# Optimization experiments

Measured on AMD Instinct MI355X. Metric: run time of the kernel, lower is better.

The kernel has to match this reference:

```python
import jax, jax.numpy as jnp
import numpy as np

B, S, D, H = 2, 2048, 1024, 16
DK = D // H
ALPHA = 0.5


def setup_inputs() -> dict:
    key = jax.random.key(0)
    ks = jax.random.split(key, 16)
    scale = 0.02
    return {
        "q": jax.random.normal(ks[0], (B, S, D), dtype=jnp.float32),
        "k": jax.random.normal(ks[1], (B, S, D), dtype=jnp.float32),
        "v": jax.random.normal(ks[2], (B, S, D), dtype=jnp.float32),
        "attn_mask": jax.random.randint(ks[3], (S, S), 0, 2, dtype=jnp.int32),
        "causal_mask": jax.random.uniform(ks[4], (S, S), dtype=jnp.float32),
        "Wq": jax.random.normal(ks[5], (D, D), dtype=jnp.float32) * scale,
        "bq": jnp.zeros((D,), dtype=jnp.float32),
        "Wk": jax.random.normal(ks[6], (D, D), dtype=jnp.float32) * scale,
        "bk": jnp.zeros((D,), dtype=jnp.float32),
        "Wv": jax.random.normal(ks[7], (D, D), dtype=jnp.float32) * scale,
        "bv": jnp.zeros((D,), dtype=jnp.float32),
        "Wo": jax.random.normal(ks[8], (D, D), dtype=jnp.float32) * scale,
        "bo": jnp.zeros((D,), dtype=jnp.float32),
    }


def _split_heads(x):
    # [B, S, D] -> [B, H, S, DK]
    return x.reshape(B, S, H, DK).transpose(0, 2, 1, 3)


def reference(q, k, v, attn_mask, causal_mask, Wq, bq, Wk, bk, Wv, bv, Wo, bo):
    qh = _split_heads(q @ Wq.T + bq)
    kh = _split_heads(k @ Wk.T + bk)
    vh = _split_heads(v @ Wv.T + bv)
    scores = jnp.einsum("bhqd,bhkd->bhqk", qh, kh) / jnp.sqrt(jnp.float32(DK))
    # additive mask: positions where attn_mask == 1 get -1e9 (broadcast [S,S] -> [B,H,S,S])
    scores = jnp.where(attn_mask[None, None] == 1, jnp.float32(-1e9), scores)
    # multiplicative causal scaling (applied AFTER the fill, as in the original)
    scores = scores * (1.0 + ALPHA * causal_mask[None, None])
    probs = jax.nn.softmax(scores, axis=-1)  # dropout is identity in eval / p=0
    attn = jnp.einsum("bhqk,bhkd->bhqd", probs, vh)  # [B, H, S, DK]
    concat = attn.transpose(0, 2, 1, 3).reshape(B, S, D)
    out = concat @ Wo.T + bo
    return (out, attn)
```

## Files before the change

### kernel.cpp

```cpp
#include <hip/hip_runtime.h>
#include <hip/hip_bf16.h>

#define NB 2
#define NS 2048
#define ND 1024
#define NH 16
#define NDK 64
#define GK 1024

using bf16_t = __hip_bfloat16;
typedef __attribute__((ext_vector_type(8))) short bf16x8;
typedef __attribute__((ext_vector_type(4))) float f32x4;
typedef unsigned short u16;
typedef unsigned int u32;

#define SC_LOG2E 0.1803368801f

static __device__ __forceinline__ u16 f2bf(float f) {
    __hip_bfloat16 h = __float2bfloat16(f);
    return *reinterpret_cast<u16*>(&h);
}

static __device__ __forceinline__ u32 cvtpk2(float a, float b) {
    u32 r;
    asm("v_cvt_pk_bf16_f32 %0, %1, %2" : "=v"(r) : "v"(a), "v"(b));
    return r;
}

#define GLDS16(gp, lp)                                                                    \
    __builtin_amdgcn_global_load_lds((const __attribute__((address_space(1))) void*)(gp), \
                                     (__attribute__((address_space(3))) void*)(lp), 16, 0, 0)

struct PrepArgs {
    const float* qkv_s[3];
    u16* qkv_d[3];
    const float* w_s[4];
    u16* w_d[4];
    const int* am;
    const float* cm;
    float* comb;
};

__global__ __launch_bounds__(256) void prep_kernel(PrepArgs a) {
    const int x = blockIdx.x, y = blockIdx.y, tid = threadIdx.x;
    if (y < 3) {
        int i = x * 256 + tid;
        float4 v = reinterpret_cast<const float4*>(a.qkv_s[y])[i];
        ushort4 o;
        o.x = f2bf(v.x); o.y = f2bf(v.y); o.z = f2bf(v.z); o.w = f2bf(v.w);
        reinterpret_cast<ushort4*>(a.qkv_d[y])[i] = o;
    } else if (y == 3) {
        int w = x >> 10;
        int i = (x & 1023) * 256 + tid;
        float4 v = reinterpret_cast<const float4*>(a.w_s[w])[i];
        ushort4 o;
        o.x = f2bf(v.x); o.y = f2bf(v.y); o.z = f2bf(v.z); o.w = f2bf(v.w);
        reinterpret_cast<ushort4*>(a.w_d[w])[i] = o;
    } else {
        int i = (x * 256 + tid) * 4;
        int4 m = *reinterpret_cast<const int4*>(a.am + i);
        float4 c = *reinterpret_cast<const float4*>(a.cm + i);
        float4 r;
        r.x = (m.x == 1) ? -1.0f : fmaf(0.5f * SC_LOG2E, c.x, SC_LOG2E);
        r.y = (m.y == 1) ? -1.0f : fmaf(0.5f * SC_LOG2E, c.y, SC_LOG2E);
        r.z = (m.z == 1) ? -1.0f : fmaf(0.5f * SC_LOG2E, c.z, SC_LOG2E);
        r.w = (m.w == 1) ? -1.0f : fmaf(0.5f * SC_LOG2E, c.w, SC_LOG2E);
        *reinterpret_cast<float4*>(a.comb + i) = r;
    }
}

struct MMArgs {
    const u16* A;
    const u16* W;
    const float* bias;
    void* out;
};

template <int BN, int MODE>
__global__ __launch_bounds__(256) void mm_glds(MMArgs g0, MMArgs g1, MMArgs g2) {
    const MMArgs ga = (blockIdx.z == 0) ? g0 : (blockIdx.z == 1) ? g1 : g2;
    constexpr int BM = 128, BK = 32;
    constexpr int JN = BN / 32;
    __shared__ __align__(16) u16 As[2][BM * BK];
    __shared__ __align__(16) u16 Bs[2][BN * BK];

    const int tid = threadIdx.x;
    const int lane = tid & 63;
    const int w = tid >> 6;
    const int wm = w >> 1, wn = w & 1;
    const int fr = lane & 15, fg = lane >> 4;
    const int bm0 = blockIdx.y * BM, bn0 = blockIdx.x * BN;

    const u16* agp = ga.A + (size_t)(bm0 + w * 32 + (lane >> 2)) * GK + (lane & 3) * 8;
    const u16* bgp = ga.W +
                     (size_t)(bn0 + w * (BN == 128 ? 32 : 16) + (lane >> 2)) * GK +
                     (lane & 3) * 8;

    f32x4 acc[4][JN];
    const f32x4 z4 = {0.f, 0.f, 0.f, 0.f};
#pragma unroll
    for (int i = 0; i < 4; ++i)
#pragma unroll
        for (int j = 0; j < JN; ++j) acc[i][j] = z4;

    {
        u16* la = &As[0][w * 1024];
        u16* lb = &Bs[0][w * (BN == 128 ? 1024 : 512)];
        GLDS16(agp, la);
        GLDS16(agp + 16 * GK, la + 512);
        if (BN == 128) {
            GLDS16(bgp, lb);
            GLDS16(bgp + 16 * GK, lb + 512);
        } else {
            GLDS16(bgp, lb);
        }
    }
    __syncthreads();

    int cur = 0;
    for (int kt = 0; kt < GK / BK; ++kt) {
        if (kt + 1 < GK / BK) {
            const int ko = (kt + 1) * BK;
            u16* la = &As[cur ^ 1][w * 1024];
            u16* lb = &Bs[cur ^ 1][w * (BN == 128 ? 1024 : 512)];
            GLDS16(agp + ko, la);
            GLDS16(agp + ko + 16 * GK, la + 512);
            if (BN == 128) {
                GLDS16(bgp + ko, lb);
                GLDS16(bgp + ko + 16 * GK, lb + 512);
            } else {
                GLDS16(bgp + ko, lb);
            }
        }
        bf16x8 af[4], bfr[JN];
#pragma unroll
        for (int i = 0; i < 4; ++i)
            af[i] = *(const bf16x8*)&As[cur][(wm * 64 + i * 16 + fr) * BK + fg * 8];
#pragma unroll
        for (int j = 0; j < JN; ++j)
            bfr[j] = *(const bf16x8*)&Bs[cur][(wn * (BN / 2) + j * 16 + fr) * BK + fg * 8];
#pragma unroll
        for (int i = 0; i < 4; ++i)
#pragma unroll
            for (int j = 0; j < JN; ++j)
                acc[i][j] = __builtin_amdgcn_mfma_f32_16x16x32_bf16(af[i], bfr[j], acc[i][j],
                                                                    0, 0, 0);
        __syncthreads();
        cur ^= 1;
    }

#pragma unroll
    for (int j = 0; j < JN; ++j) {
        const int col = bn0 + wn * (BN / 2) + j * 16 + fr;
        const float bv_ = ga.bias[col];
#pragma unroll
        for (int i = 0; i < 4; ++i) {
#pragma unroll
            for (int r = 0; r < 4; ++r) {
                const int row = bm0 + wm * 64 + i * 16 + fg * 4 + r;
                const float val = acc[i][j][r] + bv_;
                if (MODE == 1) {
                    const int b_ = row >> 11, s_ = row & (NS - 1);
                    const int h_ = col >> 6, dk = col & (NDK - 1);
                    ((bf16_t*)ga.out)[(((size_t)(b_ * NH + h_)) * NS + s_) * NDK + dk] =
                        __float2bfloat16(val);
                } else {
                    ((float*)ga.out)[(size_t)row * ND + col] = val;
                }
            }
        }
    }
}

__global__ __launch_bounds__(256) void vtrans_kernel(const u16* __restrict__ Vh,
                                                     u16* __restrict__ VhT) {
    __shared__ __align__(16) u16 T[64][72];
    const int t = threadIdx.x;
    const int bh = blockIdx.y;
    const int s0 = blockIdx.x * 64;
    const size_t boff = (size_t)bh * NS * NDK;

    const int vkp = t & 31;
    const int vdk = (t >> 5) * 8;
    int4 va = *(const int4*)(Vh + boff + (size_t)(s0 + 2 * vkp) * NDK + vdk);
    int4 vb = *(const int4*)(Vh + boff + (size_t)(s0 + 2 * vkp + 1) * NDK + vdk);
    {
        const u16* a = (const u16*)&va;
        const u16* b = (const u16*)&vb;
#pragma unroll
        for (int j = 0; j < 8; ++j) {
            u32 pk = (u32)a[j] | ((u32)b[j] << 16);
            *(u32*)&T[vdk + j][2 * vkp] = pk;
        }
    }
    __syncthreads();
    const int d = t >> 2;
    const int so = (t & 3) * 16;
    int4 o0 = *(const int4*)&T[d][so];
    int4 o1 = *(const int4*)&T[d][so + 8];
    u16* op = VhT + boff + (size_t)d * NS + s0 + so;
    *(int4*)(op) = o0;
    *(int4*)(op + 8) = o1;
}

__global__ __launch_bounds__(256) void flash_mfma(const u16* __restrict__ Qh,
                                                  const u16* __restrict__ Kh,
                                                  const u16* __restrict__ VhT,
                                                  const float* __restrict__ comb,
                                                  float* __restrict__ attnOut,
                                                  u16* __restrict__ concatOut) {
    __shared__ __align__(16) u16 Kt[2][64 * 64];
    __shared__ __align__(16) u16 Vt[2][64 * 64];
    __shared__ __align__(16) u16 Pt[4][16][64];

    const int tid = threadIdx.x;
    const int w = tid >> 6;
    const int lane = tid & 63;
    const int qc = lane & 15;
    const int g = lane >> 4;
    const int bh = blockIdx.y;
    const int b_ = bh >> 4, h_ = bh & 15;
    const int qw = blockIdx.x * 64 + w * 16;

    const size_t bhoff = (size_t)bh * NS * NDK;

    const int srow = lane >> 3;
    const int sblk = (lane & 7) ^ srow;
    const u16* kgp = Kh + bhoff + (size_t)(w * 16 + srow) * NDK + sblk * 8;
    const u16* vgp = VhT + bhoff + (size_t)(w * 16 + srow) * NS + sblk * 8;

    bf16x8 qf[2];
    {
        const u16* qp = Qh + bhoff + (size_t)(qw + qc) * NDK + g * 8;
        qf[0] = *(const bf16x8*)(qp);
        qf[1] = *(const bf16x8*)(qp + 32);
    }

    bf16x8 vones;
#pragma unroll
    for (int j = 0; j < 8; ++j) vones[j] = (short)0x3F80;

    const f32x4 z4 = {0.f, 0.f, 0.f, 0.f};
    f32x4 o[4];
    o[0] = o[1] = o[2] = o[3] = z4;
    f32x4 o_l = z4;

    const float* crow = comb + (size_t)(qw + qc) * NS;
    const int kxor = qc & 7;
    const int pxor = (qc & 7) << 4;
    char* ptrow = (char*)&Pt[w][0][0] + qc * 128;

    {
        u16* kd = &Kt[0][(w * 16) * 64];
        u16* vd = &Vt[0][(w * 16) * 64];
        GLDS16(kgp, kd);
        GLDS16(kgp + 8 * NDK, kd + 512);
        GLDS16(vgp, vd);
        GLDS16(vgp + 8 * NS, vd + 512);
    }
    float4 cpre[4];
#pragma unroll
    for (int ks = 0; ks < 4; ++ks)
        cpre[ks] = *(const float4*)(crow + ks * 16 + g * 4);
    __syncthreads();

    int cur = 0;
#pragma unroll 2
    for (int kt = 0; kt < NS; kt += 64) {
        if (kt + 64 < NS) {
            u16* kd = &Kt[cur ^ 1][(w * 16) * 64];
            u16* vd = &Vt[cur ^ 1][(w * 16) * 64];
            GLDS16(kgp + (kt + 64) * NDK, kd);
            GLDS16(kgp + (kt + 64 + 8) * NDK, kd + 512);
            GLDS16(vgp + (kt + 64), vd);
            GLDS16(vgp + 8 * NS + (kt + 64), vd + 512);
        }
        float4 cc4[4];
#pragma unroll
        for (int ks = 0; ks < 4; ++ks) cc4[ks] = cpre[ks];
        if (kt + 64 < NS) {
#pragma unroll
            for (int ks = 0; ks < 4; ++ks)
                cpre[ks] = *(const float4*)(crow + kt + 64 + ks * 16 + g * 4);
        }

        f32x4 s[4];
        s[0] = s[1] = s[2] = s[3] = z4;
        __builtin_amdgcn_s_setprio(1);
#pragma unroll
        for (int kc = 0; kc < 2; ++kc) {
#pragma unroll
            for (int ks = 0; ks < 4; ++ks) {
                bf16x8 kf = *(const bf16x8*)&Kt[cur][(ks * 16 + qc) * 64 +
                                                     (((kc << 2) | g) ^ kxor) * 8];
                s[ks] = __builtin_amdgcn_mfma_f32_16x16x32_bf16(kf, qf[kc], s[ks], 0, 0, 0);
            }
        }
        __builtin_amdgcn_s_setprio(0);

#pragma unroll
        for (int ks = 0; ks < 4; ++ks) {
            const float* cc = (const float*)&cc4[ks];
            float p0 = __builtin_amdgcn_exp2f(s[ks][0] * cc[0]);
            float p1 = __builtin_amdgcn_exp2f(s[ks][1] * cc[1]);
            float p2 = __builtin_amdgcn_exp2f(s[ks][2] * cc[2]);
            float p3 = __builtin_amdgcn_exp2f(s[ks][3] * cc[3]);
            p0 = (cc[0] < 0.f) ? 0.f : p0;
            p1 = (cc[1] < 0.f) ? 0.f : p1;
            p2 = (cc[2] < 0.f) ? 0.f : p2;
            p3 = (cc[3] < 0.f) ? 0.f : p3;
            uint2 pw;
            pw.x = cvtpk2(p0, p1);
            pw.y = cvtpk2(p2, p3);
            *(uint2*)(ptrow + ((ks * 32 + g * 8) ^ pxor)) = pw;
        }

        __builtin_amdgcn_s_setprio(1);
#pragma unroll
        for (int kc = 0; kc < 2; ++kc) {
            bf16x8 pf = *(const bf16x8*)(ptrow + ((kc * 64 + g * 16) ^ pxor));
            o_l = __builtin_amdgcn_mfma_f32_16x16x32_bf16(pf, vones, o_l, 0, 0, 0);
#pragma unroll
            for (int dsub = 0; dsub < 4; ++dsub) {
                bf16x8 vf = *(const bf16x8*)&Vt[cur][(dsub * 16 + qc) * 64 +
                                                     (((kc << 2) | g) ^ kxor) * 8];
                o[dsub] = __builtin_amdgcn_mfma_f32_16x16x32_bf16(pf, vf, o[dsub], 0, 0, 0);
            }
        }
        __builtin_amdgcn_s_setprio(0);
        __syncthreads();
        cur ^= 1;
    }

    float inv[4];
#pragma unroll
    for (int r = 0; r < 4; ++r) inv[r] = 1.0f / o_l[r];

#pragma unroll
    for (int dsub = 0; dsub < 4; ++dsub) {
#pragma unroll
        for (int r = 0; r < 4; ++r) {
            const float val = o[dsub][r] * inv[r];
            const int qg = qw + g * 4 + r;
            const int d = dsub * 16 + qc;
            attnOut[bhoff + (size_t)qg * NDK + d] = val;
            concatOut[((size_t)b_ * NS + qg) * ND + h_ * NDK + d] = f2bf(val);
        }
    }
}

extern "C" void kernel_launch(void* const* d_in, const int* in_sizes, int n_in,
                              void* d_out, int out_size, void* d_ws, size_t ws_size,
                              hipStream_t stream) {
    const float* q = (const float*)d_in[0];
    const float* k = (const float*)d_in[1];
    const float* v = (const float*)d_in[2];
    const int* am = (const int*)d_in[3];
    const float* cm = (const float*)d_in[4];
    const float* Wq = (const float*)d_in[5];
    const float* bq = (const float*)d_in[6];
    const float* Wk = (const float*)d_in[7];
    const float* bk = (const float*)d_in[8];
    const float* Wv = (const float*)d_in[9];
    const float* bv = (const float*)d_in[10];
    const float* Wo = (const float*)d_in[11];
    const float* bo = (const float*)d_in[12];

    float* out = (float*)d_out;
    float* attn_out = out + (size_t)NB * NS * ND;

    char* p = (char*)d_ws;
    float* CB = (float*)p;  p += (size_t)NS * NS * 4;
    u16* qb = (u16*)p;      p += (size_t)NB * NS * ND * 2;
    u16* kb_ = (u16*)p;     p += (size_t)NB * NS * ND * 2;
    u16* vb_ = (u16*)p;     p += (size_t)NB * NS * ND * 2;
    u16* Wqb = (u16*)p;     p += (size_t)ND * ND * 2;
    u16* Wkb = (u16*)p;     p += (size_t)ND * ND * 2;
    u16* Wvb = (u16*)p;     p += (size_t)ND * ND * 2;
    u16* Wob = (u16*)p;     p += (size_t)ND * ND * 2;
    u16* Qh = (u16*)p;      p += (size_t)NB * NS * ND * 2;
    u16* Kh = (u16*)p;      p += (size_t)NB * NS * ND * 2;
    u16* Vh = (u16*)p;      p += (size_t)NB * NS * ND * 2;
    u16* VhT = (u16*)p;     p += (size_t)NB * NS * ND * 2;
    u16* CCb = (u16*)p;     p += (size_t)NB * NS * ND * 2;

    PrepArgs pa;
    pa.qkv_s[0] = q;  pa.qkv_d[0] = qb;
    pa.qkv_s[1] = k;  pa.qkv_d[1] = kb_;
    pa.qkv_s[2] = v;  pa.qkv_d[2] = vb_;
    pa.w_s[0] = Wq;   pa.w_d[0] = Wqb;
    pa.w_s[1] = Wk;   pa.w_d[1] = Wkb;
    pa.w_s[2] = Wv;   pa.w_d[2] = Wvb;
    pa.w_s[3] = Wo;   pa.w_d[3] = Wob;
    pa.am = am;
    pa.cm = cm;
    pa.comb = CB;
    hipLaunchKernelGGL(prep_kernel, dim3(4096, 5), dim3(256), 0, stream, pa);

    MMArgs mq = {qb, Wqb, bq, (void*)Qh};
    MMArgs mk = {kb_, Wkb, bk, (void*)Kh};
    MMArgs mv = {vb_, Wvb, bv, (void*)Vh};
    hipLaunchKernelGGL((mm_glds<128, 1>), dim3(ND / 128, 4096 / 128, 3), dim3(256), 0, stream,
                       mq, mk, mv);

    hipLaunchKernelGGL(vtrans_kernel, dim3(NS / 64, NB * NH), dim3(256), 0, stream, Vh, VhT);

    hipLaunchKernelGGL(flash_mfma, dim3(NS / 64, NB * NH), dim3(256), 0, stream, Qh, Kh, VhT,
                       CB, attn_out, CCb);

    MMArgs mo = {CCb, Wob, bo, (void*)out};
    hipLaunchKernelGGL((mm_glds<64, 0>), dim3(ND / 64, 4096 / 128, 1), dim3(256), 0, stream,
                       mo, mo, mo);
}
```

Measured before the change: 195.7 us.

## Fuse V transpose into projection epilogue and load V fragments directly from global

The V projection GEMM now writes its output already transposed (per head, dk-major) through a runtime mode flag, so the separate transpose kernel and the Vh buffer go away. The attention kernel drops the shared-memory V tile and loads the V fragments for each key block straight from global memory into registers. It also replaces the prefetched mask registers with direct loads, removes the priority hints, and sets an occupancy hint of 5 blocks per SM. The intent is to save a launch and a round trip through memory for V, and to free LDS and registers for more resident blocks. In exchange, V reads are no longer staged or double-buffered, and the GEMM epilogue now branches on a runtime mode.

```diff
diff --git a/kernel.cpp b/kernel.cpp
--- a/kernel.cpp
+++ b/kernel.cpp
@@ -74,9 +74,10 @@
     const u16* W;
     const float* bias;
     void* out;
+    int mode;
 };
 
-template <int BN, int MODE>
+template <int BN>
 __global__ __launch_bounds__(256) void mm_glds(MMArgs g0, MMArgs g1, MMArgs g2) {
     const MMArgs ga = (blockIdx.z == 0) ? g0 : (blockIdx.z == 1) ? g1 : g2;
     constexpr int BM = 128, BK = 32;
@@ -153,64 +154,46 @@
     for (int j = 0; j < JN; ++j) {
         const int col = bn0 + wn * (BN / 2) + j * 16 + fr;
         const float bv_ = ga.bias[col];
-#pragma unroll
-        for (int i = 0; i < 4; ++i) {
-#pragma unroll
-            for (int r = 0; r < 4; ++r) {
-                const int row = bm0 + wm * 64 + i * 16 + fg * 4 + r;
-                const float val = acc[i][j][r] + bv_;
-                if (MODE == 1) {
-                    const int b_ = row >> 11, s_ = row & (NS - 1);
-                    const int h_ = col >> 6, dk = col & (NDK - 1);
-                    ((bf16_t*)ga.out)[(((size_t)(b_ * NH + h_)) * NS + s_) * NDK + dk] =
-                        __float2bfloat16(val);
-                } else {
-                    ((float*)ga.out)[(size_t)row * ND + col] = val;
+        if (ga.mode == 2) {
+            const int h_ = col >> 6, dk = col & (NDK - 1);
+#pragma unroll
+            for (int i = 0; i < 4; ++i) {
+                const int row0 = bm0 + wm * 64 + i * 16 + fg * 4;
+                const int b_ = row0 >> 11, s_ = row0 & (NS - 1);
+                uint2 pw;
+                pw.x = cvtpk2(acc[i][j][0] + bv_, acc[i][j][1] + bv_);
+                pw.y = cvtpk2(acc[i][j][2] + bv_, acc[i][j][3] + bv_);
+                *(uint2*)((u16*)ga.out +
+                          (((size_t)(b_ * NH + h_)) * NDK + dk) * NS + s_) = pw;
+            }
+        } else {
+#pragma unroll
+            for (int i = 0; i < 4; ++i) {
+#pragma unroll
+                for (int r = 0; r < 4; ++r) {
+                    const int row = bm0 + wm * 64 + i * 16 + fg * 4 + r;
+                    const float val = acc[i][j][r] + bv_;
+                    if (ga.mode == 1) {
+                        const int b_ = row >> 11, s_ = row & (NS - 1);
+                        const int h_ = col >> 6, dk = col & (NDK - 1);
+                        ((bf16_t*)ga.out)[(((size_t)(b_ * NH + h_)) * NS + s_) * NDK + dk] =
+                            __float2bfloat16(val);
+                    } else {
+                        ((float*)ga.out)[(size_t)row * ND + col] = val;
+                    }
                 }
             }
         }
     }
 }
 
-__global__ __launch_bounds__(256) void vtrans_kernel(const u16* __restrict__ Vh,
-                                                     u16* __restrict__ VhT) {
-    __shared__ __align__(16) u16 T[64][72];
-    const int t = threadIdx.x;
-    const int bh = blockIdx.y;
-    const int s0 = blockIdx.x * 64;
-    const size_t boff = (size_t)bh * NS * NDK;
-
-    const int vkp = t & 31;
-    const int vdk = (t >> 5) * 8;
-    int4 va = *(const int4*)(Vh + boff + (size_t)(s0 + 2 * vkp) * NDK + vdk);
-    int4 vb = *(const int4*)(Vh + boff + (size_t)(s0 + 2 * vkp + 1) * NDK + vdk);
-    {
-        const u16* a = (const u16*)&va;
-        const u16* b = (const u16*)&vb;
-#pragma unroll
-        for (int j = 0; j < 8; ++j) {
-            u32 pk = (u32)a[j] | ((u32)b[j] << 16);
-            *(u32*)&T[vdk + j][2 * vkp] = pk;
-        }
-    }
-    __syncthreads();
-    const int d = t >> 2;
-    const int so = (t & 3) * 16;
-    int4 o0 = *(const int4*)&T[d][so];
-    int4 o1 = *(const int4*)&T[d][so + 8];
-    u16* op = VhT + boff + (size_t)d * NS + s0 + so;
-    *(int4*)(op) = o0;
-    *(int4*)(op + 8) = o1;
-}
-
-__global__ __launch_bounds__(256) void flash_mfma(const u16* __restrict__ Qh,
-                                                  const u16* __restrict__ Kh,
-                                                  const u16* __restrict__ VhT,
-                                                  const float* __restrict__ comb,
-                                                  float* __restrict__ attnOut,
-                                                  u16* __restrict__ concatOut) {
+__global__ __launch_bounds__(256, 5) void flash_mfma(const u16* __restrict__ Qh,
+                                                     const u16* __restrict__ Kh,
+                                                     const u16* __restrict__ VhT,
+                                                     const float* __restrict__ comb,
+                                                     float* __restrict__ attnOut,
+                                                     u16* __restrict__ concatOut) {
     __shared__ __align__(16) u16 Kt[2][64 * 64];
-    __shared__ __align__(16) u16 Vt[2][64 * 64];
     __shared__ __align__(16) u16 Pt[4][16][64];
 
     const int tid = threadIdx.x;
@@ -227,7 +210,8 @@
     const int srow = lane >> 3;
     const int sblk = (lane & 7) ^ srow;
     const u16* kgp = Kh + bhoff + (size_t)(w * 16 + srow) * NDK + sblk * 8;
-    const u16* vgp = VhT + bhoff + (size_t)(w * 16 + srow) * NS + sblk * 8;
+
+    const u16* vbase = VhT + bhoff + (size_t)qc * NS + g * 8;
 
     bf16x8 qf[2];
     {
@@ -250,43 +234,28 @@
     const int pxor = (qc & 7) << 4;
     char* ptrow = (char*)&Pt[w][0][0] + qc * 128;
 
-    {
-        u16* kd = &Kt[0][(w * 16) * 64];
-        u16* vd = &Vt[0][(w * 16) * 64];
-        GLDS16(kgp, kd);
-        GLDS16(kgp + 8 * NDK, kd + 512);
-        GLDS16(vgp, vd);
-        GLDS16(vgp + 8 * NS, vd + 512);
-    }
-    float4 cpre[4];
-#pragma unroll
-    for (int ks = 0; ks < 4; ++ks)
-        cpre[ks] = *(const float4*)(crow + ks * 16 + g * 4);
+    GLDS16(kgp, &Kt[0][(w * 16) * 64]);
+    GLDS16(kgp + 8 * NDK, &Kt[0][(w * 16) * 64 + 512]);
     __syncthreads();
 
     int cur = 0;
-#pragma unroll 2
     for (int kt = 0; kt < NS; kt += 64) {
         if (kt + 64 < NS) {
             u16* kd = &Kt[cur ^ 1][(w * 16) * 64];
-            u16* vd = &Vt[cur ^ 1][(w * 16) * 64];
             GLDS16(kgp + (kt + 64) * NDK, kd);
             GLDS16(kgp + (kt + 64 + 8) * NDK, kd + 512);
-            GLDS16(vgp + (kt + 64), vd);
-            GLDS16(vgp + 8 * NS + (kt + 64), vd + 512);
-        }
-        float4 cc4[4];
-#pragma unroll
-        for (int ks = 0; ks < 4; ++ks) cc4[ks] = cpre[ks];
-        if (kt + 64 < NS) {
-#pragma unroll
-            for (int ks = 0; ks < 4; ++ks)
-                cpre[ks] = *(const float4*)(crow + kt + 64 + ks * 16 + g * 4);
-        }
+        }
+
+        bf16x8 vf[2][4];
+#pragma unroll
+        for (int kc = 0; kc < 2; ++kc)
+#pragma unroll
+            for (int dsub = 0; dsub < 4; ++dsub)
+                vf[kc][dsub] =
+                    *(const bf16x8*)(vbase + (size_t)dsub * 16 * NS + kt + kc * 32);
 
         f32x4 s[4];
         s[0] = s[1] = s[2] = s[3] = z4;
-        __builtin_amdgcn_s_setprio(1);
 #pragma unroll
         for (int kc = 0; kc < 2; ++kc) {
 #pragma unroll
@@ -296,11 +265,11 @@
                 s[ks] = __builtin_amdgcn_mfma_f32_16x16x32_bf16(kf, qf[kc], s[ks], 0, 0, 0);
             }
         }
-        __builtin_amdgcn_s_setprio(0);
 
 #pragma unroll
         for (int ks = 0; ks < 4; ++ks) {
-            const float* cc = (const float*)&cc4[ks];
+            float4 c4 = *(const float4*)(crow + kt + ks * 16 + g * 4);
+            const float* cc = (const float*)&c4;
             float p0 = __builtin_amdgcn_exp2f(s[ks][0] * cc[0]);
             float p1 = __builtin_amdgcn_exp2f(s[ks][1] * cc[1]);
             float p2 = __builtin_amdgcn_exp2f(s[ks][2] * cc[2]);
@@ -315,19 +284,15 @@
             *(uint2*)(ptrow + ((ks * 32 + g * 8) ^ pxor)) = pw;
         }
 
-        __builtin_amdgcn_s_setprio(1);
 #pragma unroll
         for (int kc = 0; kc < 2; ++kc) {
             bf16x8 pf = *(const bf16x8*)(ptrow + ((kc * 64 + g * 16) ^ pxor));
             o_l = __builtin_amdgcn_mfma_f32_16x16x32_bf16(pf, vones, o_l, 0, 0, 0);
 #pragma unroll
-            for (int dsub = 0; dsub < 4; ++dsub) {
-                bf16x8 vf = *(const bf16x8*)&Vt[cur][(dsub * 16 + qc) * 64 +
-                                                     (((kc << 2) | g) ^ kxor) * 8];
-                o[dsub] = __builtin_amdgcn_mfma_f32_16x16x32_bf16(pf, vf, o[dsub], 0, 0, 0);
-            }
-        }
-        __builtin_amdgcn_s_setprio(0);
+            for (int dsub = 0; dsub < 4; ++dsub)
+                o[dsub] =
+                    __builtin_amdgcn_mfma_f32_16x16x32_bf16(pf, vf[kc][dsub], o[dsub], 0, 0, 0);
+        }
         __syncthreads();
         cur ^= 1;
     }
@@ -380,7 +345,6 @@
     u16* Wob = (u16*)p;     p += (size_t)ND * ND * 2;
     u16* Qh = (u16*)p;      p += (size_t)NB * NS * ND * 2;
     u16* Kh = (u16*)p;      p += (size_t)NB * NS * ND * 2;
-    u16* Vh = (u16*)p;      p += (size_t)NB * NS * ND * 2;
     u16* VhT = (u16*)p;     p += (size_t)NB * NS * ND * 2;
     u16* CCb = (u16*)p;     p += (size_t)NB * NS * ND * 2;
 
@@ -397,18 +361,16 @@
     pa.comb = CB;
     hipLaunchKernelGGL(prep_kernel, dim3(4096, 5), dim3(256), 0, stream, pa);
 
-    MMArgs mq = {qb, Wqb, bq, (void*)Qh};
-    MMArgs mk = {kb_, Wkb, bk, (void*)Kh};
-    MMArgs mv = {vb_, Wvb, bv, (void*)Vh};
-    hipLaunchKernelGGL((mm_glds<128, 1>), dim3(ND / 128, 4096 / 128, 3), dim3(256), 0, stream,
+    MMArgs mq = {qb, Wqb, bq, (void*)Qh, 1};
+    MMArgs mk = {kb_, Wkb, bk, (void*)Kh, 1};
+    MMArgs mv = {vb_, Wvb, bv, (void*)VhT, 2};
+    hipLaunchKernelGGL((mm_glds<128>), dim3(ND / 128, 4096 / 128, 3), dim3(256), 0, stream,
                        mq, mk, mv);
-
-    hipLaunchKernelGGL(vtrans_kernel, dim3(NS / 64, NB * NH), dim3(256), 0, stream, Vh, VhT);
 
     hipLaunchKernelGGL(flash_mfma, dim3(NS / 64, NB * NH), dim3(256), 0, stream, Qh, Kh, VhT,
                        CB, attn_out, CCb);
 
-    MMArgs mo = {CCb, Wob, bo, (void*)out};
-    hipLaunchKernelGGL((mm_glds<64, 0>), dim3(ND / 64, 4096 / 128, 1), dim3(256), 0, stream,
+    MMArgs mo = {CCb, Wob, bo, (void*)out, 0};
+    hipLaunchKernelGGL((mm_glds<64>), dim3(ND / 64, 4096 / 128, 1), dim3(256), 0, stream,
                        mo, mo, mo);
 }
```

Result: slower. 275.6 us (+40.8%).
